# Kernel optimization log

Hardware: AMD Instinct MI355X
Metric: run time of the kernel (lower is better)

## Reference

```python
import jax, jax.numpy as jnp
import numpy as np

B, S, D = 2, 2048, 2560
H, HKV, HD = 8, 4, 256
EPS = 1e-6
SCALING = 256 ** -0.5          # query_pre_attn_scalar ** -0.5
SOFTCAP = 4096.0               # sliding_window passed positionally into softcap slot
NEG = -1e9


def rms_norm(x, w):
    # x: [..., HD]; computed in fp32 like the torch module
    xf = x.astype(jnp.float32)
    out = xf * jax.lax.rsqrt(jnp.mean(xf * xf, axis=-1, keepdims=True) + EPS)
    return (out * (1.0 + w.astype(jnp.float32))).astype(x.dtype)


def rotate_half(x):
    x1, x2 = x[..., : HD // 2], x[..., HD // 2:]
    return jnp.concatenate((-x2, x1), axis=-1)


def apply_rope(x, cos, sin):
    # cos/sin: [B, S, HD] -> broadcast over head axis 1
    c, s = cos[:, None], sin[:, None]
    return x * c + rotate_half(x) * s


def setup_inputs() -> dict:
    key = jax.random.key(0)
    ks = jax.random.split(key, 6)
    x = jax.random.normal(ks[0], (B, S, D), dtype=jnp.float32)
    # RoPE angles (theta=10000, linear scaling factor 8)
    inv_freq = 1.0 / (10000.0 ** (np.arange(0, HD, 2, dtype=np.float32) / HD))
    pos = np.arange(S, dtype=np.float32) / 8.0
    ang = np.einsum('s,d->sd', pos, inv_freq)
    ang = np.concatenate([ang, ang], axis=-1)               # [S, HD]
    cos = jnp.asarray(np.broadcast_to(np.cos(ang), (B, S, HD)).copy())
    sin = jnp.asarray(np.broadcast_to(np.sin(ang), (B, S, HD)).copy())
    # causal additive mask [B, 1, S, S]
    causal = np.where(np.tril(np.ones((S, S), dtype=bool)), 0.0, NEG).astype(np.float32)
    mask = jnp.asarray(np.broadcast_to(causal, (B, 1, S, S)).copy())
    sc = 0.02
    q_w = jax.random.normal(ks[1], (H * HD, D), dtype=jnp.float32) * sc
    k_w = jax.random.normal(ks[2], (HKV * HD, D), dtype=jnp.float32) * sc
    v_w = jax.random.normal(ks[3], (HKV * HD, D), dtype=jnp.float32) * sc
    o_w = jax.random.normal(ks[4], (D, H * HD), dtype=jnp.float32) * sc
    qn_w = jnp.zeros((HD,), dtype=jnp.float32)
    kn_w = jnp.zeros((HD,), dtype=jnp.float32)
    return {"x": x, "cos": cos, "sin": sin, "mask": mask,
            "q_w": q_w, "k_w": k_w, "v_w": v_w, "o_w": o_w,
            "qn_w": qn_w, "kn_w": kn_w}


def reference(x, cos, sin, mask, q_w, k_w, v_w, o_w, qn_w, kn_w):
    b, s, _ = x.shape
    # projections -> [B, H(kv), S, HD]
    q = (x @ q_w.T).reshape(b, s, H, HD).transpose(0, 2, 1, 3)
    k = (x @ k_w.T).reshape(b, s, HKV, HD).transpose(0, 2, 1, 3)
    v = (x @ v_w.T).reshape(b, s, HKV, HD).transpose(0, 2, 1, 3)
    q = rms_norm(q, qn_w)
    k = rms_norm(k, kn_w)
    q = apply_rope(q, cos, sin)
    k = apply_rope(k, cos, sin)
    # GQA: repeat kv heads (interleave matches repeat_interleave on dim=1)
    rep = H // HKV
    k = jnp.repeat(k, rep, axis=1)
    v = jnp.repeat(v, rep, axis=1)
    w = jnp.einsum('bhqd,bhkd->bhqk', q, k) * SCALING
    w = jnp.tanh(w / SOFTCAP) * SOFTCAP                     # softcap (bug-faithful)
    w = w + mask[:, :, :, : k.shape[2]]
    p = jax.nn.softmax(w.astype(jnp.float32), axis=-1).astype(q.dtype)
    attn = jnp.einsum('bhqk,bhkd->bhqd', p, v)
    attn = attn.transpose(0, 2, 1, 3).reshape(b, s, H * HD)
    return attn @ o_w.T
```

## Files before the change

kernel.cpp:

```cpp
#include <hip/hip_runtime.h>
#include <hip/hip_bf16.h>

#define BB   2
#define SS   2048
#define DD   2560
#define HH   8
#define HKVV 4
#define HDD  256
#define MM   (BB*SS)
#define NQ   (HH*HDD)
#define NKV  (HKVV*HDD)
#define SCALING 0.0625f
#define SOFTCAP 4096.0f
#define CAPC    (1.0f/(3.0f*SOFTCAP*SOFTCAP))
#define M0      20.0f

typedef __attribute__((ext_vector_type(8))) short short8;
typedef __attribute__((ext_vector_type(8))) unsigned short ushort8;
typedef __attribute__((ext_vector_type(4))) unsigned short us4;
typedef __attribute__((ext_vector_type(4))) float f32x4;

__device__ __forceinline__ float bf2f(unsigned short u) {
    union { unsigned int i; float f; } v; v.i = ((unsigned int)u) << 16; return v.f;
}
__device__ __forceinline__ unsigned short f2bf(float f) {
    union { float f; unsigned int i; } v; v.f = f;
    return (unsigned short)((v.i + 0x7fffu + ((v.i >> 16) & 1u)) >> 16);
}
__device__ __forceinline__ f32x4 mfma16(short8 a, short8 b, f32x4 c) {
    return __builtin_amdgcn_mfma_f32_16x16x32_bf16(a, b, c, 0, 0, 0);
}

__device__ __forceinline__ void async_cp16(const void* g, void* l) {
    __builtin_amdgcn_global_load_lds(
        (__attribute__((address_space(1))) void*)(g),
        (__attribute__((address_space(3))) void*)(l), 16, 0, 0);
}

__device__ __forceinline__ ushort8 ld8(const unsigned short* p) { return *(const ushort8*)p; }
__device__ __forceinline__ ushort8 ld8(const float* p) {
    ushort8 r;
#pragma unroll
    for (int i = 0; i < 8; i++) r[i] = f2bf(p[i]);
    return r;
}
__device__ __forceinline__ void stc(float* p, float v)          { *p = v; }
__device__ __forceinline__ void stc(unsigned short* p, float v) { *p = f2bf(v); }
__device__ __forceinline__ void stage8(const unsigned short* src, unsigned short* lds) {
    async_cp16(src, lds);
}
__device__ __forceinline__ void stage8(const float* src, unsigned short* lds) {
    *(ushort8*)lds = ld8(src);
}

__global__ __launch_bounds__(256) void cvt_bf16(const float* __restrict__ in,
                                                unsigned short* __restrict__ out, int n4)
{
    int i = blockIdx.x * 256 + threadIdx.x;
    const int stride = gridDim.x * 256;
    for (; i < n4; i += stride) {
        float4 v = ((const float4*)in)[i];
        us4 o;
        o[0] = f2bf(v.x); o[1] = f2bf(v.y); o[2] = f2bf(v.z); o[3] = f2bf(v.w);
        ((us4*)out)[i] = o;
    }
}

__global__ __launch_bounds__(256) void cvt_w4(const float* __restrict__ s0,
                                              const float* __restrict__ s1,
                                              const float* __restrict__ s2,
                                              const float* __restrict__ s3,
                                              unsigned short* __restrict__ dst)
{
    const int y = blockIdx.y;
    const int n4q = (int)((size_t)NQ  * DD / 4);
    const int n4k = (int)((size_t)NKV * DD / 4);
    const float* src; int n4; size_t off4;
    if (y == 0)      { src = s0; n4 = n4q; off4 = 0; }
    else if (y == 1) { src = s1; n4 = n4k; off4 = (size_t)n4q; }
    else if (y == 2) { src = s2; n4 = n4k; off4 = (size_t)n4q + n4k; }
    else             { src = s3; n4 = n4q; off4 = (size_t)n4q + 2 * (size_t)n4k; }
    us4* out = (us4*)dst + off4;
    int i = blockIdx.x * 256 + threadIdx.x;
    const int stride = gridDim.x * 256;
    for (; i < n4; i += stride) {
        float4 v = ((const float4*)src)[i];
        us4 o;
        o[0] = f2bf(v.x); o[1] = f2bf(v.y); o[2] = f2bf(v.z); o[3] = f2bf(v.w);
        out[i] = o;
    }
}

template<typename TA, typename TB, typename TC, bool VT_OUT>
__global__ __launch_bounds__(256) void gemm_k(const TA* __restrict__ A,
                                              const TB* __restrict__ Bm,
                                              TC* __restrict__ C,
                                              int M, int N, int K)
{
    __shared__ __align__(16) unsigned short As[128][32];
    __shared__ __align__(16) unsigned short Bs[128][32];

    const int tid  = threadIdx.x;
    const int bm   = blockIdx.x, bn = blockIdx.y;
    const int wave = tid >> 6, lane = tid & 63;
    const int quad = lane >> 4, lm = lane & 15;
    const int wm = (wave >> 1) * 64, wn = (wave & 1) * 64;

    f32x4 acc[4][4];
#pragma unroll
    for (int i = 0; i < 4; i++)
#pragma unroll
        for (int j = 0; j < 4; j++) acc[i][j] = (f32x4)0.0f;

    unsigned short* AsF = &As[0][0];
    unsigned short* BsF = &Bs[0][0];
    const int grow = tid >> 2;
    const int gcol = (tid & 3) * 8;
    const TA* Ab = A  + (size_t)(bm * 128) * K;
    const TB* Bb = Bm + (size_t)(bn * 128) * K;

    for (int k0 = 0; k0 < K; k0 += 32) {
        stage8(&Ab[(size_t)(grow     ) * K + k0 + gcol], AsF + tid * 8);
        stage8(&Ab[(size_t)(grow + 64) * K + k0 + gcol], AsF + 2048 + tid * 8);
        stage8(&Bb[(size_t)(grow     ) * K + k0 + gcol], BsF + tid * 8);
        stage8(&Bb[(size_t)(grow + 64) * K + k0 + gcol], BsF + 2048 + tid * 8);
        __syncthreads();

        short8 af[4], bf[4];
#pragma unroll
        for (int t = 0; t < 4; t++) af[t] = *(const short8*)&As[wm + t * 16 + lm][quad * 8];
#pragma unroll
        for (int t = 0; t < 4; t++) bf[t] = *(const short8*)&Bs[wn + t * 16 + lm][quad * 8];
#pragma unroll
        for (int i = 0; i < 4; i++)
#pragma unroll
            for (int j = 0; j < 4; j++)
                acc[i][j] = mfma16(af[i], bf[j], acc[i][j]);
        __syncthreads();
    }

#pragma unroll
    for (int i = 0; i < 4; i++)
#pragma unroll
        for (int j = 0; j < 4; j++) {
            if constexpr (VT_OUT) {
                int row0 = bm * 128 + wm + i * 16 + quad * 4;
                int col  = bn * 128 + wn + j * 16 + lm;
                int b    = row0 >> 11, s0 = row0 & (SS - 1);
                int kvh  = col >> 8,   d  = col & (HDD - 1);
                us4 pk;
#pragma unroll
                for (int r = 0; r < 4; r++) pk[r] = f2bf(acc[i][j][r]);
                *(us4*)&C[(((size_t)b * HKVV + kvh) * HDD + d) * SS + s0] = pk;
            } else {
#pragma unroll
                for (int r = 0; r < 4; r++) {
                    int row = bm * 128 + wm + i * 16 + quad * 4 + r;
                    int col = bn * 128 + wn + j * 16 + lm;
                    stc(&C[(size_t)row * N + col], acc[i][j][r]);
                }
            }
        }
}

template<int ROUTE>
__global__ __launch_bounds__(512, 2) void gemm256(const unsigned short* __restrict__ A,
                                                  const unsigned short* __restrict__ Bm,
                                                  unsigned short* __restrict__ Qo,
                                                  unsigned short* __restrict__ Ko,
                                                  unsigned short* __restrict__ Vo,
                                                  float* __restrict__ Cf,
                                                  int K)
{
    __shared__ __align__(16) unsigned short Asm[2][256 * 64];
    __shared__ __align__(16) unsigned short Bsm[2][256 * 64];

    const int tid  = threadIdx.x;
    const int wid  = tid >> 6, lane = tid & 63;
    const int quad = lane >> 4, lm = lane & 15;
    const int wr   = wid >> 2, wc = wid & 3;
    const int bm   = blockIdx.x, bn = blockIdx.y;

    f32x4 acc[8][4];
#pragma unroll
    for (int i = 0; i < 8; i++)
#pragma unroll
        for (int j = 0; j < 4; j++) acc[i][j] = (f32x4)0.0f;

    const unsigned short* Ab = A  + (size_t)(bm * 256) * K;
    const unsigned short* Bb = Bm + (size_t)(bn * 256) * K;

    auto STAGE1 = [&](int buf, int k0, int p) {
        const int slot = (p & 3) * 512 + tid;
        const int row = slot >> 3, ch = slot & 7;
        if (p < 4)
            async_cp16(&Ab[(size_t)row * K + k0 + ((ch ^ (row & 7)) * 8)],
                       &Asm[buf][slot * 8]);
        else
            async_cp16(&Bb[(size_t)row * K + k0 + ((ch ^ (row & 7)) * 8)],
                       &Bsm[buf][slot * 8]);
    };

#define LOAD_A(MH)                                                                \
    _Pragma("unroll")                                                             \
    for (int mi = 0; mi < 4; mi++) {                                              \
        const int arow = wr * 128 + ((MH) * 4 + mi) * 16 + lm;                    \
        _Pragma("unroll")                                                         \
        for (int ks = 0; ks < 2; ks++)                                            \
            a_[mi][ks] = *(const short8*)&Asm[cur][arow * 64 +                    \
                            (((ks * 4 + quad) ^ (arow & 7)) * 8)];                \
    }
#define LOAD_B(NH)                                                                \
    _Pragma("unroll")                                                             \
    for (int ni = 0; ni < 2; ni++) {                                              \
        const int brow = wc * 64 + ((NH) * 2 + ni) * 16 + lm;                     \
        _Pragma("unroll")                                                         \
        for (int ks = 0; ks < 2; ks++)                                            \
            b_[ni][ks] = *(const short8*)&Bsm[cur][brow * 64 +                    \
                            (((ks * 4 + quad) ^ (brow & 7)) * 8)];                \
    }
#define MFMA_PH(MH, NH)                                                           \
    asm volatile("s_waitcnt lgkmcnt(0)" ::: "memory");                            \
    __builtin_amdgcn_sched_barrier(0);                                            \
    __builtin_amdgcn_s_setprio(1);                                                \
    _Pragma("unroll")                                                             \
    for (int mi = 0; mi < 4; mi++)                                                \
        _Pragma("unroll")                                                         \
        for (int ni = 0; ni < 2; ni++)                                            \
            _Pragma("unroll")                                                     \
            for (int ks = 0; ks < 2; ks++)                                        \
                acc[(MH) * 4 + mi][(NH) * 2 + ni] =                               \
                    mfma16(a_[mi][ks], b_[ni][ks],                                \
                           acc[(MH) * 4 + mi][(NH) * 2 + ni]);                    \
    __builtin_amdgcn_s_setprio(0);                                                \
    __builtin_amdgcn_sched_barrier(0);

    const int NT = K >> 6;
#pragma unroll
    for (int p = 0; p < 8; p++) STAGE1(0, 0, p);
    int cur = 0;

    for (int t = 0; t < NT; t++) {
        const bool more = (t + 1 < NT);
        const int nb = cur ^ 1, nk = (t + 1) * 64;

        if (more) {
            STAGE1(nb, nk, 0); STAGE1(nb, nk, 1);
            asm volatile("s_waitcnt vmcnt(2)" ::: "memory");
        } else {
            asm volatile("s_waitcnt vmcnt(0)" ::: "memory");
        }
        __builtin_amdgcn_s_barrier();
        __builtin_amdgcn_sched_barrier(0);

        short8 a_[4][2], b_[2][2];
        LOAD_A(0) LOAD_B(0) MFMA_PH(0, 0)
        if (more) { STAGE1(nb, nk, 2); STAGE1(nb, nk, 3); }
        LOAD_B(1)           MFMA_PH(0, 1)
        if (more) { STAGE1(nb, nk, 4); STAGE1(nb, nk, 5); }
        LOAD_A(1)           MFMA_PH(1, 1)
        if (more) { STAGE1(nb, nk, 6); STAGE1(nb, nk, 7); }
        LOAD_B(0)           MFMA_PH(1, 0)

        __builtin_amdgcn_s_barrier();
        __builtin_amdgcn_sched_barrier(0);
        cur ^= 1;
    }
#undef LOAD_A
#undef LOAD_B
#undef MFMA_PH

    if constexpr (ROUTE == 1) {
#pragma unroll
        for (int m = 0; m < 8; m++)
#pragma unroll
            for (int n = 0; n < 4; n++) {
                const int row0 = bm * 256 + wr * 128 + m * 16 + quad * 4;
                const int col  = bn * 256 + wc * 64 + n * 16 + lm;
#pragma unroll
                for (int r = 0; r < 4; r++)
                    Cf[(size_t)(row0 + r) * DD + col] = acc[m][n][r];
            }
    } else if (bn < 8) {
#pragma unroll
        for (int m = 0; m < 8; m++)
#pragma unroll
            for (int n = 0; n < 4; n++) {
                const int row0 = bm * 256 + wr * 128 + m * 16 + quad * 4;
                const int colg = bn * 256 + wc * 64 + n * 16 + lm;
#pragma unroll
                for (int r = 0; r < 4; r++)
                    Qo[(size_t)(row0 + r) * NQ + colg] = f2bf(acc[m][n][r]);
            }
    } else if (bn < 12) {
#pragma unroll
        for (int m = 0; m < 8; m++)
#pragma unroll
            for (int n = 0; n < 4; n++) {
                const int row0 = bm * 256 + wr * 128 + m * 16 + quad * 4;
                const int ck   = bn * 256 + wc * 64 + n * 16 + lm - 2048;
#pragma unroll
                for (int r = 0; r < 4; r++)
                    Ko[(size_t)(row0 + r) * NKV + ck] = f2bf(acc[m][n][r]);
            }
    } else {
#pragma unroll
        for (int m = 0; m < 8; m++)
#pragma unroll
            for (int n = 0; n < 4; n++) {
                const int row0 = bm * 256 + wr * 128 + m * 16 + quad * 4;
                const int cv   = bn * 256 + wc * 64 + n * 16 + lm - 3072;
                const int b = row0 >> 11, s0 = row0 & (SS - 1);
                const int kvh = cv >> 8, d = cv & (HDD - 1);
                us4 pk;
#pragma unroll
                for (int r = 0; r < 4; r++) pk[r] = f2bf(acc[m][n][r]);
                *(us4*)&Vo[(((size_t)b * HKVV + kvh) * HDD + d) * SS + s0] = pk;
            }
    }
}

template<typename TA>
__global__ __launch_bounds__(256) void gemm_qkv(const TA* __restrict__ A,
                                                const unsigned short* __restrict__ Bm,
                                                unsigned short* __restrict__ Qo,
                                                unsigned short* __restrict__ Ko,
                                                unsigned short* __restrict__ Vo,
                                                int K)
{
    __shared__ __align__(16) unsigned short As[128][32];
    __shared__ __align__(16) unsigned short Bs[128][32];

    const int tid  = threadIdx.x;
    const int bm   = blockIdx.x, bn = blockIdx.y;
    const int wave = tid >> 6, lane = tid & 63;
    const int quad = lane >> 4, lm = lane & 15;
    const int wm = (wave >> 1) * 64, wn = (wave & 1) * 64;

    f32x4 acc[4][4];
#pragma unroll
    for (int i = 0; i < 4; i++)
#pragma unroll
        for (int j = 0; j < 4; j++) acc[i][j] = (f32x4)0.0f;

    unsigned short* AsF = &As[0][0];
    unsigned short* BsF = &Bs[0][0];
    const int grow = tid >> 2;
    const int gcol = (tid & 3) * 8;
    const TA* Ab = A  + (size_t)(bm * 128) * K;
    const unsigned short* Bb = Bm + (size_t)(bn * 128) * K;

    for (int k0 = 0; k0 < K; k0 += 32) {
        stage8(&Ab[(size_t)(grow     ) * K + k0 + gcol], AsF + tid * 8);
        stage8(&Ab[(size_t)(grow + 64) * K + k0 + gcol], AsF + 2048 + tid * 8);
        stage8(&Bb[(size_t)(grow     ) * K + k0 + gcol], BsF + tid * 8);
        stage8(&Bb[(size_t)(grow + 64) * K + k0 + gcol], BsF + 2048 + tid * 8);
        __syncthreads();

        short8 af[4], bf[4];
#pragma unroll
        for (int t = 0; t < 4; t++) af[t] = *(const short8*)&As[wm + t * 16 + lm][quad * 8];
#pragma unroll
        for (int t = 0; t < 4; t++) bf[t] = *(const short8*)&Bs[wn + t * 16 + lm][quad * 8];
#pragma unroll
        for (int i = 0; i < 4; i++)
#pragma unroll
            for (int j = 0; j < 4; j++)
                acc[i][j] = mfma16(af[i], bf[j], acc[i][j]);
        __syncthreads();
    }

#pragma unroll
    for (int i = 0; i < 4; i++)
#pragma unroll
        for (int j = 0; j < 4; j++) {
            const int row0 = bm * 128 + wm + i * 16 + quad * 4;
            const int col  = bn * 128 + wn + j * 16 + lm;
            if (col < 2048) {
#pragma unroll
                for (int r = 0; r < 4; r++)
                    Qo[(size_t)(row0 + r) * NQ + col] = f2bf(acc[i][j][r]);
            } else if (col < 3072) {
                const int ck = col - 2048;
#pragma unroll
                for (int r = 0; r < 4; r++)
                    Ko[(size_t)(row0 + r) * NKV + ck] = f2bf(acc[i][j][r]);
            } else {
                const int cv = col - 3072;
                const int b = row0 >> 11, s0 = row0 & (SS - 1);
                const int kvh = cv >> 8, d = cv & (HDD - 1);
                us4 pk;
#pragma unroll
                for (int r = 0; r < 4; r++) pk[r] = f2bf(acc[i][j][r]);
                *(us4*)&Vo[(((size_t)b * HKVV + kvh) * HDD + d) * SS + s0] = pk;
            }
        }
}

__global__ __launch_bounds__(256) void norm_rope2(unsigned short* __restrict__ Qx,
                                                  unsigned short* __restrict__ Kx,
                                                  const float* __restrict__ qnw,
                                                  const float* __restrict__ knw,
                                                  const float* __restrict__ cosb,
                                                  const float* __restrict__ sinb)
{
    const int bs = blockIdx.x;
    const int y  = blockIdx.y;
    const int t  = threadIdx.x;
    unsigned short* X; const float* nw; int nheads, h;
    if (y < HH) { X = Qx; nw = qnw; nheads = HH;   h = y; }
    else        { X = Kx; nw = knw; nheads = HKVV; h = y - HH; }

    __shared__ float xs[256];
    __shared__ float red[4];

    const size_t base = ((size_t)bs * nheads + h) * HDD;
    float v = bf2f(X[base + t]);
    xs[t] = v;

    float p = v * v;
#pragma unroll
    for (int off = 32; off >= 1; off >>= 1) p += __shfl_xor(p, off);
    if ((t & 63) == 0) red[t >> 6] = p;
    __syncthreads();
    float sum = red[0] + red[1] + red[2] + red[3];
    float rs  = rsqrtf(sum * (1.0f / HDD) + 1e-6f);

    const int pt = (t + 128) & 255;
    float w1 = 1.0f + nw[t];
    float w2 = 1.0f + nw[pt];
    float normed  = v * rs * w1;
    float partner = xs[pt] * rs * w2;
    float rot = (t < 128) ? -partner : partner;
    float c = cosb[(size_t)bs * HDD + t];
    float s = sinb[(size_t)bs * HDD + t];
    X[base + t] = f2bf(normed * c + rot * s);
}

__global__ __launch_bounds__(256) void norm_rope(unsigned short* __restrict__ X,
                                                 const float* __restrict__ nw,
                                                 const float* __restrict__ cosb,
                                                 const float* __restrict__ sinb,
                                                 int nheads)
{
    const int bs = blockIdx.x;
    const int h  = blockIdx.y;
    const int t  = threadIdx.x;

    __shared__ float xs[256];
    __shared__ float red[4];

    const size_t base = ((size_t)bs * nheads + h) * HDD;
    float v = bf2f(X[base + t]);
    xs[t] = v;

    float p = v * v;
#pragma unroll
    for (int off = 32; off >= 1; off >>= 1) p += __shfl_xor(p, off);
    if ((t & 63) == 0) red[t >> 6] = p;
    __syncthreads();
    float sum = red[0] + red[1] + red[2] + red[3];
    float rs  = rsqrtf(sum * (1.0f / HDD) + 1e-6f);

    const int pt = (t + 128) & 255;
    float w1 = 1.0f + nw[t];
    float w2 = 1.0f + nw[pt];
    float normed  = v * rs * w1;
    float partner = xs[pt] * rs * w2;
    float rot = (t < 128) ? -partner : partner;
    float c = cosb[(size_t)bs * HDD + t];
    float s = sinb[(size_t)bs * HDD + t];
    X[base + t] = f2bf(normed * c + rot * s);
}

__device__ const unsigned char unit_tbl[48] = {
    62, 124, 125, 120, 121,
    58, 116, 117, 112, 113,
    54, 108, 109, 104, 105,
    50, 100, 101,  96,  97,
    46,  92,  93,  88,  89,
    42,  84,  85,  80,  81,
    38,  76,  77,  72,  73,
    34,  68,  69,  64,  65,
    30,  26,  22,  18,  14, 10, 6, 2
};

__global__ __launch_bounds__(256) void attn_split(const unsigned short* __restrict__ Q,
                                                  const unsigned short* __restrict__ K,
                                                  const unsigned short* __restrict__ VT,
                                                  unsigned short* __restrict__ O,
                                                  float* __restrict__ Opart,
                                                  float* __restrict__ lpart)
{
    const int tid = threadIdx.x, w = tid >> 6, lane = tid & 63;
    const int quad = lane >> 4, lm = lane & 15;
    const int hb = blockIdx.x;
    const int h = hb & 7, b = hb >> 3, kvh = h >> 1;

    const unsigned int u = unit_tbl[blockIdx.y];
    const int qb = u >> 2;
    const bool single = (u & 2) != 0;
    const int half = u & 1;
    const int q0 = qb * 64;
    const int T  = 2 * (qb + 1);
    const int t_lo = (!single && half) ? (qb + 1) : 0;
    const int t_hi = single ? T : (half ? T : (qb + 1));

    __shared__ __align__(16) unsigned short Ks[2][32 * 256];
    __shared__ __align__(16) unsigned short Vt[256 * 32];
    __shared__ __align__(16) unsigned short Ps[4 * 512];

    const unsigned short* Qb = Q + (((size_t)b * SS + q0 + w * 16 + lm) * HH + h) * HDD;
    short8 qf[8];
#pragma unroll
    for (int c = 0; c < 8; c++) qf[c] = *(const short8*)&Qb[c * 32 + quad * 8];

    const unsigned short* Kb = K  + (size_t)b * SS * NKV + (size_t)kvh * HDD;
    const unsigned short* Vb = VT + ((size_t)b * HKVV + kvh) * HDD * (size_t)SS;

    f32x4 o_acc[16];
#pragma unroll
    for (int i = 0; i < 16; i++) o_acc[i] = (f32x4)0.0f;
    float l_r[4] = {0.f, 0.f, 0.f, 0.f};

    const int mylo = q0 + w * 16;
    const int row  = mylo + quad * 4;

    auto STAGE_K = [&](int bi, int k0) {
#pragma unroll
        for (int p = 0; p < 4; p++) {
            const int slot = p * 256 + tid;
            const int krow = slot >> 5, kc = slot & 31;
            async_cp16(&Kb[(size_t)(k0 + krow) * NKV + ((kc ^ (krow & 7)) * 8)],
                       &Ks[bi][slot * 8]);
        }
    };
    auto STAGE_V = [&](int k0) {
#pragma unroll
        for (int p = 0; p < 4; p++) {
            const int slot = p * 256 + tid;
            const int vd = slot >> 2, vc = slot & 3;
            async_cp16(&Vb[(size_t)vd * SS + k0 + ((vc ^ ((vd >> 1) & 3)) * 8)],
                       &Vt[slot * 8]);
        }
    };

    STAGE_K(0, t_lo * 32);
    STAGE_V(t_lo * 32);
    int cur = 0;

    for (int t = t_lo; t < t_hi; t++) {
        const int k0 = t * 32;
        const bool more = (t + 1 < t_hi);

        if (more) {
            STAGE_K(cur ^ 1, k0 + 32);
            asm volatile("s_waitcnt vmcnt(8)" ::: "memory");
        } else {
            asm volatile("s_waitcnt vmcnt(4)" ::: "memory");
        }
        __builtin_amdgcn_s_barrier();
        __builtin_amdgcn_sched_barrier(0);

        short8 pf;
        if (k0 <= mylo + 15) {
            f32x4 sa0 = (f32x4)0.0f, sa1 = (f32x4)0.0f;
            __builtin_amdgcn_s_setprio(1);
#pragma unroll
            for (int c = 0; c < 8; c++) {
                const int cs = (((c * 4 + quad) ^ (lm & 7))) * 8;
                short8 kf0 = *(const short8*)&Ks[cur][lm * 256 + cs];
                short8 kf1 = *(const short8*)&Ks[cur][(16 + lm) * 256 + cs];
                sa0 = mfma16(qf[c], kf0, sa0);
                sa1 = mfma16(qf[c], kf1, sa1);
            }
            __builtin_amdgcn_s_setprio(0);

            const bool msk = (k0 + 31 > mylo);
            float pe[2][4];
#pragma unroll
            for (int t2 = 0; t2 < 2; t2++) {
                const int key = k0 + t2 * 16 + lm;
#pragma unroll
                for (int r = 0; r < 4; r++) {
                    float s = (t2 ? sa1[r] : sa0[r]) * SCALING;
                    s = s - s * s * s * CAPC;
                    float e = __expf(s - M0);
                    if (msk && key > row + r) e = 0.0f;
                    pe[t2][r] = e;
                    l_r[r] += e;
                }
            }

#pragma unroll
            for (int t2 = 0; t2 < 2; t2++)
#pragma unroll
                for (int r = 0; r < 4; r++) {
                    const int g = (t2 * 2 + (lm >> 3)) ^ r ^ quad;
                    Ps[w * 512 + (quad * 4 + r) * 32 + g * 8 + (lm & 7)] = f2bf(pe[t2][r]);
                }
            asm volatile("s_waitcnt lgkmcnt(0)" ::: "memory");
            __builtin_amdgcn_sched_barrier(0);
            const int gr = quad ^ (lm & 3) ^ (lm >> 2);
            pf = *(const short8*)&Ps[w * 512 + lm * 32 + gr * 8];
        }

        if (more) asm volatile("s_waitcnt vmcnt(4)" ::: "memory");
        else      asm volatile("s_waitcnt vmcnt(0)" ::: "memory");
        __builtin_amdgcn_s_barrier();
        __builtin_amdgcn_sched_barrier(0);

        if (k0 <= mylo + 15) {
            __builtin_amdgcn_s_setprio(1);
#pragma unroll
            for (int nt = 0; nt < 16; nt++) {
                short8 vf = *(const short8*)&Vt[(nt * 16 + lm) * 32
                                                + ((quad ^ ((lm >> 1) & 3)) * 8)];
                o_acc[nt] = mfma16(pf, vf, o_acc[nt]);
            }
            __builtin_amdgcn_s_setprio(0);
        }

        __builtin_amdgcn_sched_barrier(0);
        __builtin_amdgcn_s_barrier();
        __builtin_amdgcn_sched_barrier(0);
        if (more) STAGE_V(k0 + 32);
        cur ^= 1;
    }

#pragma unroll
    for (int off = 1; off < 16; off <<= 1)
#pragma unroll
        for (int r = 0; r < 4; r++) l_r[r] += __shfl_xor(l_r[r], off);

    if (single) {
#pragma unroll
        for (int r = 0; r < 4; r++) {
            float inv = 1.0f / l_r[r];
            unsigned short* Ob = O + ((size_t)b * SS + row + r) * NQ + h * HDD;
#pragma unroll
            for (int nt = 0; nt < 16; nt++)
                Ob[nt * 16 + lm] = f2bf(o_acc[nt][r] * inv);
        }
    } else {
        const int slot = (((b * HH + h) * 16 + (qb - 16)) << 1) | half;
        float* Ob = Opart + ((size_t)slot * 64 + w * 16 + quad * 4) * 256;
#pragma unroll
        for (int r = 0; r < 4; r++) {
            if (lm == 0) lpart[slot * 64 + w * 16 + quad * 4 + r] = l_r[r];
#pragma unroll
            for (int nt = 0; nt < 16; nt++)
                Ob[(size_t)r * 256 + nt * 16 + lm] = o_acc[nt][r];
        }
    }
}

__global__ __launch_bounds__(256) void attn_reduce(const float* __restrict__ Op,
                                                   const float* __restrict__ lp,
                                                   unsigned short* __restrict__ ATT)
{
    const int sp  = blockIdx.x >> 4;
    const int wr0 = (blockIdx.x & 15) * 4;
    const int r   = threadIdx.x >> 6;
    const int c0  = (threadIdx.x & 63) * 4;
    const int wrow = wr0 + r;
    const int qbm = sp & 15, h = (sp >> 4) & 7, b = sp >> 7;

    const size_t base0 = ((size_t)(sp * 2) * 64 + wrow) * 256;
    const size_t base1 = base0 + (size_t)64 * 256;
    float4 a = *(const float4*)&Op[base0 + c0];
    float4 d = *(const float4*)&Op[base1 + c0];
    float l = lp[sp * 2 * 64 + wrow] + lp[(sp * 2 + 1) * 64 + wrow];
    float inv = 1.0f / l;
    us4 o;
    o[0] = f2bf((a.x + d.x) * inv); o[1] = f2bf((a.y + d.y) * inv);
    o[2] = f2bf((a.z + d.z) * inv); o[3] = f2bf((a.w + d.w) * inv);
    const int srow = (16 + qbm) * 64 + wrow;
    *(us4*)&ATT[(((size_t)b * SS + srow) * HH + h) * HDD + c0] = o;
}

__global__ __launch_bounds__(256) void attn_kernel(const unsigned short* __restrict__ Q,
                                                   const unsigned short* __restrict__ K,
                                                   const unsigned short* __restrict__ VT,
                                                   unsigned short* __restrict__ O)
{
    const int tid = threadIdx.x, w = tid >> 6, lane = tid & 63;
    const int quad = lane >> 4, lm = lane & 15;
    const int h = blockIdx.y, b = blockIdx.z, kvh = h >> 1;

    const int bx = blockIdx.x;
    const int qb = (bx & 1) ? (31 - (bx >> 1)) : (bx >> 1);
    const int q0 = qb * 64;
    const int T  = 2 * (qb + 1);

    __shared__ __align__(16) unsigned short Ks[2][32 * 256];
    __shared__ __align__(16) unsigned short Vt[2][256 * 32];
    __shared__ __align__(16) unsigned short Ps[4 * 512];

    const unsigned short* Qb = Q + (((size_t)b * SS + q0 + w * 16 + lm) * HH + h) * HDD;
    short8 qf[8];
#pragma unroll
    for (int c = 0; c < 8; c++) qf[c] = *(const short8*)&Qb[c * 32 + quad * 8];

    const unsigned short* Kb = K  + (size_t)b * SS * NKV + (size_t)kvh * HDD;
    const unsigned short* Vb = VT + ((size_t)b * HKVV + kvh) * HDD * (size_t)SS;

    f32x4 o_acc[16];
#pragma unroll
    for (int i = 0; i < 16; i++) o_acc[i] = (f32x4)0.0f;
    float l_r[4] = {0.f, 0.f, 0.f, 0.f};

    const int mylo = q0 + w * 16;
    const int row  = mylo + quad * 4;

    auto STAGE = [&](int bi, int k0) {
#pragma unroll
        for (int p = 0; p < 4; p++) {
            const int slot = p * 256 + tid;
            const int krow = slot >> 5, kc = slot & 31;
            async_cp16(&Kb[(size_t)(k0 + krow) * NKV + ((kc ^ (krow & 7)) * 8)],
                       &Ks[bi][slot * 8]);
            const int vd = slot >> 2, vc = slot & 3;
            async_cp16(&Vb[(size_t)vd * SS + k0 + ((vc ^ ((vd >> 1) & 3)) * 8)],
                       &Vt[bi][slot * 8]);
        }
    };

    STAGE(0, 0);
    int cur = 0;

    for (int t = 0; t < T; t++) {
        const int k0 = t * 32;

        if (t + 1 < T) {
            STAGE(cur ^ 1, k0 + 32);
            asm volatile("s_waitcnt vmcnt(8)" ::: "memory");
        } else {
            asm volatile("s_waitcnt vmcnt(0)" ::: "memory");
        }
        __builtin_amdgcn_s_barrier();
        __builtin_amdgcn_sched_barrier(0);

        if (k0 <= mylo + 15) {
            f32x4 sa0 = (f32x4)0.0f, sa1 = (f32x4)0.0f;
            __builtin_amdgcn_s_setprio(1);
#pragma unroll
            for (int c = 0; c < 8; c++) {
                const int cs = (((c * 4 + quad) ^ (lm & 7))) * 8;
                short8 kf0 = *(const short8*)&Ks[cur][lm * 256 + cs];
                short8 kf1 = *(const short8*)&Ks[cur][(16 + lm) * 256 + cs];
                sa0 = mfma16(qf[c], kf0, sa0);
                sa1 = mfma16(qf[c], kf1, sa1);
            }
            __builtin_amdgcn_s_setprio(0);

            const bool msk = (k0 + 31 > mylo);
            float pe[2][4];
#pragma unroll
            for (int t2 = 0; t2 < 2; t2++) {
                const int key = k0 + t2 * 16 + lm;
#pragma unroll
                for (int r = 0; r < 4; r++) {
                    float s = (t2 ? sa1[r] : sa0[r]) * SCALING;
                    s = s - s * s * s * CAPC;
                    float e = __expf(s - M0);
                    if (msk && key > row + r) e = 0.0f;
                    pe[t2][r] = e;
                    l_r[r] += e;
                }
            }

#pragma unroll
            for (int t2 = 0; t2 < 2; t2++)
#pragma unroll
                for (int r = 0; r < 4; r++) {
                    const int g = (t2 * 2 + (lm >> 3)) ^ r ^ quad;
                    Ps[w * 512 + (quad * 4 + r) * 32 + g * 8 + (lm & 7)] = f2bf(pe[t2][r]);
                }
            asm volatile("s_waitcnt lgkmcnt(0)" ::: "memory");
            __builtin_amdgcn_sched_barrier(0);
            const int gr = quad ^ (lm & 3) ^ (lm >> 2);
            short8 pf = *(const short8*)&Ps[w * 512 + lm * 32 + gr * 8];

            __builtin_amdgcn_s_setprio(1);
#pragma unroll
            for (int nt = 0; nt < 16; nt++) {
                short8 vf = *(const short8*)&Vt[cur][(nt * 16 + lm) * 32
                                                    + ((quad ^ ((lm >> 1) & 3)) * 8)];
                o_acc[nt] = mfma16(pf, vf, o_acc[nt]);
            }
            __builtin_amdgcn_s_setprio(0);
        }

        __builtin_amdgcn_sched_barrier(0);
        __builtin_amdgcn_s_barrier();
        __builtin_amdgcn_sched_barrier(0);
        cur ^= 1;
    }

#pragma unroll
    for (int off = 1; off < 16; off <<= 1)
#pragma unroll
        for (int r = 0; r < 4; r++) l_r[r] += __shfl_xor(l_r[r], off);
#pragma unroll
    for (int r = 0; r < 4; r++) {
        float inv = 1.0f / l_r[r];
        unsigned short* Ob = O + ((size_t)b * SS + row + r) * NQ + h * HDD;
#pragma unroll
        for (int nt = 0; nt < 16; nt++)
            Ob[nt * 16 + lm] = f2bf(o_acc[nt][r] * inv);
    }
}

extern "C" void kernel_launch(void* const* d_in, const int* in_sizes, int n_in,
                              void* d_out, int out_size, void* d_ws, size_t ws_size,
                              hipStream_t stream)
{
    const float* x    = (const float*)d_in[0];
    const float* cosb = (const float*)d_in[1];
    const float* sinb = (const float*)d_in[2];
    const float* q_w  = (const float*)d_in[4];
    const float* k_w  = (const float*)d_in[5];
    const float* v_w  = (const float*)d_in[6];
    const float* o_w  = (const float*)d_in[7];
    const float* qn_w = (const float*)d_in[8];
    const float* kn_w = (const float*)d_in[9];
    float* out = (float*)d_out;

    const size_t sz_xb = (size_t)MM * DD;
    const size_t sz_wq = (size_t)NQ * DD;
    const size_t sz_wk = (size_t)NKV * DD;
    const size_t sz_q  = (size_t)MM * NQ;
    const size_t sz_k  = (size_t)MM * NKV;

    const size_t needA = (sz_xb + 2 * sz_wq + 2 * sz_wk + sz_q + 2 * sz_k) * 2;
    const size_t needB = (2 * sz_wq + 2 * sz_wk + sz_q + 2 * sz_k) * 2;

    if (ws_size >= needA) {
        unsigned short* xb  = (unsigned short*)d_ws;
        unsigned short* wqb = xb  + sz_xb;
        unsigned short* wkb = wqb + sz_wq;
        unsigned short* wvb = wkb + sz_wk;
        unsigned short* wob = wvb + sz_wk;
        unsigned short* Qw  = wob + sz_wq;
        unsigned short* Kw  = Qw  + sz_q;
        unsigned short* VTw = Kw  + sz_k;
        float* Opart = (float*)d_ws;
        float* lpart = Opart + (size_t)512 * 64 * 256;
        unsigned short* ATT = Qw;

        cvt_bf16<<<2048, 256, 0, stream>>>(x, xb, (int)(sz_xb / 4));
        cvt_w4<<<dim3(512, 4), 256, 0, stream>>>(q_w, k_w, v_w, o_w, wqb);

        gemm256<0><<<dim3(MM/256, 4096/256), 512, 0, stream>>>(
            xb, wqb, Qw, Kw, VTw, nullptr, DD);

        norm_rope2<<<dim3(MM, HH + HKVV), 256, 0, stream>>>(Qw, Kw, qn_w, kn_w, cosb, sinb);

        attn_split<<<dim3(16, 48), 256, 0, stream>>>(Qw, Kw, VTw, ATT, Opart, lpart);
        attn_reduce<<<4096, 256, 0, stream>>>(Opart, lpart, ATT);

        gemm256<1><<<dim3(MM/256, DD/256), 512, 0, stream>>>(
            ATT, wob, nullptr, nullptr, nullptr, out, NQ);
    } else if (ws_size >= needB) {
        unsigned short* wqb = (unsigned short*)d_ws;
        unsigned short* wkb = wqb + sz_wq;
        unsigned short* wvb = wkb + sz_wk;
        unsigned short* wob = wvb + sz_wk;
        unsigned short* Qw  = wob + sz_wq;
        unsigned short* Kw  = Qw  + sz_q;
        unsigned short* VTw = Kw  + sz_k;
        unsigned short* ATT = wqb;

        cvt_w4<<<dim3(512, 4), 256, 0, stream>>>(q_w, k_w, v_w, o_w, wqb);

        gemm_qkv<float>
            <<<dim3(MM/128, 4096/128), 256, 0, stream>>>(x, wqb, Qw, Kw, VTw, DD);

        norm_rope2<<<dim3(MM, HH + HKVV), 256, 0, stream>>>(Qw, Kw, qn_w, kn_w, cosb, sinb);

        attn_kernel<<<dim3(32, HH, BB), 256, 0, stream>>>(Qw, Kw, VTw, ATT);

        gemm_k<unsigned short, unsigned short, float, false>
            <<<dim3(MM/128, DD/128), 256, 0, stream>>>(ATT, wob, out, MM, DD, NQ);
    } else {
        unsigned short* Qw  = (unsigned short*)d_ws;
        unsigned short* Kw  = Qw  + sz_q;
        unsigned short* VTw = Kw  + sz_k;
        unsigned short* ATT = VTw + sz_k;

        gemm_k<float, float, unsigned short, false>
            <<<dim3(MM/128, NQ /128), 256, 0, stream>>>(x, q_w, Qw,  MM, NQ,  DD);
        gemm_k<float, float, unsigned short, false>
            <<<dim3(MM/128, NKV/128), 256, 0, stream>>>(x, k_w, Kw,  MM, NKV, DD);
        gemm_k<float, float, unsigned short, true>
            <<<dim3(MM/128, NKV/128), 256, 0, stream>>>(x, v_w, VTw, MM, NKV, DD);

        norm_rope<<<dim3(MM, HH),   256, 0, stream>>>(Qw, qn_w, cosb, sinb, HH);
        norm_rope<<<dim3(MM, HKVV), 256, 0, stream>>>(Kw, kn_w, cosb, sinb, HKVV);

        attn_kernel<<<dim3(32, HH, BB), 256, 0, stream>>>(Qw, Kw, VTw, ATT);

        gemm_k<unsigned short, float, float, false>
            <<<dim3(MM/128, DD/128), 256, 0, stream>>>(ATT, o_w, out, MM, DD, NQ);
    }
}
```

Before: 471.1 us.

## Deepen gemm256 pipeline to four 32-wide K stages; use 128-tile GEMM for output projection

The 256x256 GEMM kernel switches from a double-buffered K=64 tile with interleaved partial stage loads to a four-buffer ring of K=32 tiles, prefetching three stages ahead, with a new XOR swizzle for the narrower rows. Each stage now loads all A/B fragments then issues one block of 32 MFMAs. The output projection launch is changed from gemm256 to the existing 128x128 gemm_k kernel, giving more blocks for the N=2560 output. This trades finer-grained intra-stage overlap and halved K per barrier (twice as many barriers) for deeper prefetch; the output projection change aims at better occupancy/wave count.

```diff
diff --git a/kernel.cpp b/kernel.cpp
--- a/kernel.cpp
+++ b/kernel.cpp
@@ -172,8 +172,8 @@
                                                   float* __restrict__ Cf,
                                                   int K)
 {
-    __shared__ __align__(16) unsigned short Asm[2][256 * 64];
-    __shared__ __align__(16) unsigned short Bsm[2][256 * 64];
+    __shared__ __align__(16) unsigned short Asm[4][256 * 32];
+    __shared__ __align__(16) unsigned short Bsm[4][256 * 32];
 
     const int tid  = threadIdx.x;
     const int wid  = tid >> 6, lane = tid & 63;
@@ -190,85 +190,69 @@
     const unsigned short* Ab = A  + (size_t)(bm * 256) * K;
     const unsigned short* Bb = Bm + (size_t)(bn * 256) * K;
 
-    auto STAGE1 = [&](int buf, int k0, int p) {
-        const int slot = (p & 3) * 512 + tid;
-        const int row = slot >> 3, ch = slot & 7;
-        if (p < 4)
-            async_cp16(&Ab[(size_t)row * K + k0 + ((ch ^ (row & 7)) * 8)],
-                       &Asm[buf][slot * 8]);
-        else
-            async_cp16(&Bb[(size_t)row * K + k0 + ((ch ^ (row & 7)) * 8)],
-                       &Bsm[buf][slot * 8]);
+    auto STAGE = [&](int buf, int k0) {
+#pragma unroll
+        for (int p = 0; p < 2; p++) {
+            const int slot = p * 512 + tid;
+            const int row = slot >> 2, ch = slot & 3;
+            const int sc = ch ^ ((row >> 1) & 3);
+            async_cp16(&Ab[(size_t)row * K + k0 + sc * 8], &Asm[buf][slot * 8]);
+        }
+#pragma unroll
+        for (int p = 0; p < 2; p++) {
+            const int slot = p * 512 + tid;
+            const int row = slot >> 2, ch = slot & 3;
+            const int sc = ch ^ ((row >> 1) & 3);
+            async_cp16(&Bb[(size_t)row * K + k0 + sc * 8], &Bsm[buf][slot * 8]);
+        }
     };
 
-#define LOAD_A(MH)                                                                \
-    _Pragma("unroll")                                                             \
-    for (int mi = 0; mi < 4; mi++) {                                              \
-        const int arow = wr * 128 + ((MH) * 4 + mi) * 16 + lm;                    \
-        _Pragma("unroll")                                                         \
-        for (int ks = 0; ks < 2; ks++)                                            \
-            a_[mi][ks] = *(const short8*)&Asm[cur][arow * 64 +                    \
-                            (((ks * 4 + quad) ^ (arow & 7)) * 8)];                \
-    }
-#define LOAD_B(NH)                                                                \
-    _Pragma("unroll")                                                             \
-    for (int ni = 0; ni < 2; ni++) {                                              \
-        const int brow = wc * 64 + ((NH) * 2 + ni) * 16 + lm;                     \
-        _Pragma("unroll")                                                         \
-        for (int ks = 0; ks < 2; ks++)                                            \
-            b_[ni][ks] = *(const short8*)&Bsm[cur][brow * 64 +                    \
-                            (((ks * 4 + quad) ^ (brow & 7)) * 8)];                \
-    }
-#define MFMA_PH(MH, NH)                                                           \
-    asm volatile("s_waitcnt lgkmcnt(0)" ::: "memory");                            \
-    __builtin_amdgcn_sched_barrier(0);                                            \
-    __builtin_amdgcn_s_setprio(1);                                                \
-    _Pragma("unroll")                                                             \
-    for (int mi = 0; mi < 4; mi++)                                                \
-        _Pragma("unroll")                                                         \
-        for (int ni = 0; ni < 2; ni++)                                            \
-            _Pragma("unroll")                                                     \
-            for (int ks = 0; ks < 2; ks++)                                        \
-                acc[(MH) * 4 + mi][(NH) * 2 + ni] =                               \
-                    mfma16(a_[mi][ks], b_[ni][ks],                                \
-                           acc[(MH) * 4 + mi][(NH) * 2 + ni]);                    \
-    __builtin_amdgcn_s_setprio(0);                                                \
-    __builtin_amdgcn_sched_barrier(0);
-
-    const int NT = K >> 6;
-#pragma unroll
-    for (int p = 0; p < 8; p++) STAGE1(0, 0, p);
-    int cur = 0;
-
-    for (int t = 0; t < NT; t++) {
-        const bool more = (t + 1 < NT);
-        const int nb = cur ^ 1, nk = (t + 1) * 64;
-
-        if (more) {
-            STAGE1(nb, nk, 0); STAGE1(nb, nk, 1);
-            asm volatile("s_waitcnt vmcnt(2)" ::: "memory");
+    const int NT = K >> 5;
+    STAGE(0, 0); STAGE(1, 32); STAGE(2, 64);
+
+    for (int s = 0; s < NT; s++) {
+        const int cur = s & 3;
+        const int rem = NT - 1 - s;
+
+        if (rem >= 3) {
+            STAGE((s + 3) & 3, (s + 3) * 32);
+            asm volatile("s_waitcnt vmcnt(12)" ::: "memory");
+        } else if (rem == 2) {
+            asm volatile("s_waitcnt vmcnt(8)" ::: "memory");
+        } else if (rem == 1) {
+            asm volatile("s_waitcnt vmcnt(4)" ::: "memory");
         } else {
             asm volatile("s_waitcnt vmcnt(0)" ::: "memory");
         }
         __builtin_amdgcn_s_barrier();
         __builtin_amdgcn_sched_barrier(0);
 
-        short8 a_[4][2], b_[2][2];
-        LOAD_A(0) LOAD_B(0) MFMA_PH(0, 0)
-        if (more) { STAGE1(nb, nk, 2); STAGE1(nb, nk, 3); }
-        LOAD_B(1)           MFMA_PH(0, 1)
-        if (more) { STAGE1(nb, nk, 4); STAGE1(nb, nk, 5); }
-        LOAD_A(1)           MFMA_PH(1, 1)
-        if (more) { STAGE1(nb, nk, 6); STAGE1(nb, nk, 7); }
-        LOAD_B(0)           MFMA_PH(1, 0)
-
+        short8 a_[8], b_[4];
+#pragma unroll
+        for (int mi = 0; mi < 8; mi++) {
+            const int arow = wr * 128 + mi * 16 + lm;
+            a_[mi] = *(const short8*)&Asm[cur][arow * 32 +
+                        ((quad ^ ((arow >> 1) & 3)) * 8)];
+        }
+#pragma unroll
+        for (int ni = 0; ni < 4; ni++) {
+            const int brow = wc * 64 + ni * 16 + lm;
+            b_[ni] = *(const short8*)&Bsm[cur][brow * 32 +
+                        ((quad ^ ((brow >> 1) & 3)) * 8)];
+        }
+        asm volatile("s_waitcnt lgkmcnt(0)" ::: "memory");
+        __builtin_amdgcn_sched_barrier(0);
+        __builtin_amdgcn_s_setprio(1);
+#pragma unroll
+        for (int mi = 0; mi < 8; mi++)
+#pragma unroll
+            for (int ni = 0; ni < 4; ni++)
+                acc[mi][ni] = mfma16(a_[mi], b_[ni], acc[mi][ni]);
+        __builtin_amdgcn_s_setprio(0);
+        __builtin_amdgcn_sched_barrier(0);
         __builtin_amdgcn_s_barrier();
         __builtin_amdgcn_sched_barrier(0);
-        cur ^= 1;
-    }
-#undef LOAD_A
-#undef LOAD_B
-#undef MFMA_PH
+    }
 
     if constexpr (ROUTE == 1) {
 #pragma unroll
@@ -860,8 +844,8 @@
         attn_split<<<dim3(16, 48), 256, 0, stream>>>(Qw, Kw, VTw, ATT, Opart, lpart);
         attn_reduce<<<4096, 256, 0, stream>>>(Opart, lpart, ATT);
 
-        gemm256<1><<<dim3(MM/256, DD/256), 512, 0, stream>>>(
-            ATT, wob, nullptr, nullptr, nullptr, out, NQ);
+        gemm_k<unsigned short, unsigned short, float, false>
+            <<<dim3(MM/128, DD/128), 256, 0, stream>>>(ATT, wob, out, MM, DD, NQ);
     } else if (ws_size >= needB) {
         unsigned short* wqb = (unsigned short*)d_ws;
         unsigned short* wkb = wqb + sz_wq;
```

Result: no change. 463.5 us (-1.6%).
